# Performance work log

Hardware: AMD Instinct MI355X
Metric: run time of the kernel (lower is better)

The kernel has to match this reference:

```python
import jax, jax.numpy as jnp
import numpy as np

L, H, D, C, V, B, T, BLOCK = 6, 12, 64, 768, 32000, 2, 1024, 2048
EPS = 1e-5


def setup_inputs() -> dict:
    key = jax.random.key(0)
    ks = jax.random.split(key, 21)
    s = 0.02
    n = lambda k, shape: (jax.random.normal(k, shape, dtype=jnp.float32) * s)
    return {
        "x": jax.random.randint(ks[0], (B, T), 0, V),
        "tok_emb": n(ks[1], (V, C)),
        "pos_emb": n(ks[2], (BLOCK, C)),
        "Wq": n(ks[3], (L, H, C, D)),
        "Wk": n(ks[4], (L, H, C, D)),
        "Wv": n(ks[5], (L, H, C, D)),
        "Wo": n(ks[6], (L, H * D, C)),
        "bo": jnp.zeros((L, C), jnp.float32),
        "ln1_g": jnp.ones((L, C), jnp.float32),
        "ln1_b": jnp.zeros((L, C), jnp.float32),
        "ln2_g": jnp.ones((L, C), jnp.float32),
        "ln2_b": jnp.zeros((L, C), jnp.float32),
        "W1": n(ks[7], (L, C, 4 * C)),
        "b1": jnp.zeros((L, 4 * C), jnp.float32),
        "W2": n(ks[8], (L, 4 * C, C)),
        "b2": jnp.zeros((L, C), jnp.float32),
        "lnf_g": jnp.ones((C,), jnp.float32),
        "lnf_b": jnp.zeros((C,), jnp.float32),
        "Wh": n(ks[9], (C, V)),
        "bh": jnp.zeros((V,), jnp.float32),
    }


def _layernorm(x, g, b):
    m = jnp.mean(x, axis=-1, keepdims=True)
    v = jnp.mean(jnp.square(x - m), axis=-1, keepdims=True)
    return (x - m) * jax.lax.rsqrt(v + EPS) * g + b


def _forward(x, tok_emb, pos_emb, Wq, Wk, Wv, Wo, bo, ln1_g, ln1_b, ln2_g, ln2_b,
             W1, b1, W2, b2, lnf_g, lnf_b, Wh, bh):
    h = tok_emb[x] + pos_emb[:T]  # (B,T,C)
    causal = jnp.tril(jnp.ones((T, T), bool))
    scale = C ** (-0.5)  # NOTE: source scales by n_embd**-0.5, not head_size
    for l in range(L):
        a_in = _layernorm(h, ln1_g[l], ln1_b[l])
        q = jnp.einsum('btc,hcd->bhtd', a_in, Wq[l])
        k = jnp.einsum('btc,hcd->bhtd', a_in, Wk[l])
        v = jnp.einsum('btc,hcd->bhtd', a_in, Wv[l])
        scores = jnp.einsum('bhtd,bhsd->bhts', q, k) * scale
        scores = jnp.where(causal, scores, -jnp.inf)
        w = jax.nn.softmax(scores, axis=-1)
        o = jnp.einsum('bhts,bhsd->bhtd', w, v)  # (B,H,T,D)
        o = o.transpose(0, 2, 1, 3).reshape(B, T, H * D)
        h = h + o @ Wo[l] + bo[l]
        f_in = _layernorm(h, ln2_g[l], ln2_b[l])
        h = h + jax.nn.relu(f_in @ W1[l] + b1[l]) @ W2[l] + b2[l]
    h = _layernorm(h, lnf_g, lnf_b)
    return h @ Wh + bh  # logits (B,T,V)


def reference(x, tok_emb, pos_emb, Wq, Wk, Wv, Wo, bo, ln1_g, ln1_b, ln2_g, ln2_b,
              W1, b1, W2, b2, lnf_g, lnf_b, Wh, bh):
    return _forward(x, tok_emb, pos_emb, Wq, Wk, Wv, Wo, bo, ln1_g, ln1_b, ln2_g,
                    ln2_b, W1, b1, W2, b2, lnf_g, lnf_b, Wh, bh)
```

## Files before the change

kernel.cpp:

```cpp
#include <hip/hip_runtime.h>
#include <stdint.h>

typedef unsigned short ushortT;
typedef __bf16 bf16_t;
typedef __bf16 bf16x8 __attribute__((ext_vector_type(8)));
typedef float  f32x4  __attribute__((ext_vector_type(4)));

constexpr int N_LAYER = 6;
constexpr int N_HEAD  = 12;
constexpr int HEAD_D  = 64;
constexpr int N_EMB   = 768;
constexpr int N_VOCAB = 32000;
constexpr int N_B     = 2;
constexpr int N_T     = 1024;
constexpr int N_M     = N_B * N_T;
constexpr int QKVW    = 3 * N_EMB;
constexpr float LN_EPS = 1e-5f;
constexpr float ATT_SCALE = 0.03608439182435161f;

__device__ __forceinline__ float us2f(ushortT u) {
    union { unsigned int i; float f; } c; c.i = ((unsigned int)u) << 16; return c.f;
}
__device__ __forceinline__ ushortT f2b(float f) {
    union { float f; unsigned int u; } c; c.f = f;
    unsigned int u = c.u;
    return (ushortT)((u + 0x7fffu + ((u >> 16) & 1u)) >> 16);
}
__device__ __forceinline__ float ldw(const void* p, int isf, size_t i) {
    if (isf) return ((const float*)p)[i];
    return us2f(((const ushortT*)p)[i]);
}
__device__ __forceinline__ void gload16(const void* g, void* l) {
    __builtin_amdgcn_global_load_lds(
        (const unsigned int __attribute__((address_space(1)))*)g,
        (unsigned int __attribute__((address_space(3)))*)l, 16, 0, 0);
}

__global__ __launch_bounds__(256) void detect_kernel(const unsigned int* __restrict__ w,
                                                     int* __restrict__ flag)
{
    __shared__ int red[256];
    int cnt = 0;
    for (int i = threadIdx.x; i < 4096; i += 256) {
        unsigned int u = w[i];
        float flo = us2f((ushortT)(u & 0xffffu));
        float fhi = us2f((ushortT)(u >> 16));
        if (!(fabsf(flo) < 0.5f)) cnt++;
        if (!(fabsf(fhi) < 0.5f)) cnt++;
    }
    red[threadIdx.x] = cnt;
    __syncthreads();
    for (int off = 128; off > 0; off >>= 1) {
        if (threadIdx.x < off) red[threadIdx.x] += red[threadIdx.x + off];
        __syncthreads();
    }
    if (threadIdx.x == 0) flag[0] = (red[0] > 64) ? 1 : 0;
}

__global__ __launch_bounds__(256) void embed_kernel(const int* __restrict__ x,
        const void* __restrict__ tok, const void* __restrict__ pos,
        const int* __restrict__ flag, float* __restrict__ h)
{
    const int isf = *flag;
    int idx = blockIdx.x * 256 + threadIdx.x;
    if (idx >= N_M * N_EMB) return;
    int m = idx / N_EMB, c = idx - m * N_EMB;
    int t = m & (N_T - 1);
    int tokid = x[m];
    h[idx] = ldw(tok, isf, (size_t)tokid * N_EMB + c) + ldw(pos, isf, (size_t)t * N_EMB + c);
}

__global__ __launch_bounds__(256) void ln_kernel(const float* __restrict__ in,
        const void* __restrict__ g, const void* __restrict__ b, size_t gofs,
        const int* __restrict__ flag, ushortT* __restrict__ outHi, ushortT* __restrict__ outLo)
{
    __shared__ float red[256];
    const int isf = *flag;
    const int tid = threadIdx.x;
    const float* row = in + (size_t)blockIdx.x * N_EMB;
    float v0 = row[tid], v1 = row[tid + 256], v2 = row[tid + 512];
    red[tid] = v0 + v1 + v2;
    __syncthreads();
    for (int off = 128; off > 0; off >>= 1) {
        if (tid < off) red[tid] += red[tid + off];
        __syncthreads();
    }
    float mean = red[0] * (1.0f / N_EMB);
    __syncthreads();
    float d0 = v0 - mean, d1 = v1 - mean, d2 = v2 - mean;
    red[tid] = d0 * d0 + d1 * d1 + d2 * d2;
    __syncthreads();
    for (int off = 128; off > 0; off >>= 1) {
        if (tid < off) red[tid] += red[tid + off];
        __syncthreads();
    }
    float inv = rsqrtf(red[0] * (1.0f / N_EMB) + LN_EPS);
    size_t ob = (size_t)blockIdx.x * N_EMB;
    float dd[3] = {d0, d1, d2};
    #pragma unroll
    for (int e = 0; e < 3; e++) {
        int c = tid + e * 256;
        float v = dd[e] * inv * ldw(g, isf, gofs + c) + ldw(b, isf, gofs + c);
        ushortT hb = f2b(v);
        outHi[ob + c] = hb;
        outLo[ob + c] = f2b(v - us2f(hb));
    }
}

__global__ __launch_bounds__(256) void conv_t(const void* __restrict__ src, size_t sofs,
        const int* __restrict__ flag, ushortT* __restrict__ out, int K, int N)
{
    __shared__ float t[32][33];
    const int isf = *flag;
    const int n0 = blockIdx.x * 32, k0 = blockIdx.y * 32;
    const int tx = threadIdx.x & 31, ty = threadIdx.x >> 5;
    #pragma unroll
    for (int kk = ty; kk < 32; kk += 8)
        t[kk][tx] = ldw(src, isf, sofs + (size_t)(k0 + kk) * N + n0 + tx);
    __syncthreads();
    #pragma unroll
    for (int nn = ty; nn < 32; nn += 8)
        out[(size_t)(n0 + nn) * K + k0 + tx] = f2b(t[tx][nn]);
}

__global__ __launch_bounds__(256) void conv_qkv(const void* __restrict__ Wq,
        const void* __restrict__ Wk, const void* __restrict__ Wv, size_t wofs,
        const int* __restrict__ flag, ushortT* __restrict__ out)
{
    __shared__ float t[32][33];
    const int isf = *flag;
    const int n0 = blockIdx.x * 32, k0 = blockIdx.y * 32;
    const int which = n0 / N_EMB, rem = n0 - which * N_EMB;
    const int h = rem >> 6, d0 = rem & 63;
    const void* src = (which == 0) ? Wq : (which == 1 ? Wk : Wv);
    const size_t base = wofs + (size_t)h * N_EMB * HEAD_D;
    const int tx = threadIdx.x & 31, ty = threadIdx.x >> 5;
    #pragma unroll
    for (int kk = ty; kk < 32; kk += 8)
        t[kk][tx] = ldw(src, isf, base + (size_t)(k0 + kk) * HEAD_D + d0 + tx);
    __syncthreads();
    #pragma unroll
    for (int nn = ty; nn < 32; nn += 8)
        out[(size_t)(n0 + nn) * N_EMB + k0 + tx] = f2b(t[tx][nn]);
}

template<int BM, int BN>
__global__ __launch_bounds__(256, 2) void gemm_mfma(
    const ushortT* __restrict__ Ahi, const ushortT* __restrict__ Alo,
    const ushortT* __restrict__ Bw,
    const void* __restrict__ bias, size_t biasOfs,
    const float* resid,
    float* outF, ushortT* outHi, ushortT* outLo, void* outFinal,
    const int* __restrict__ flag, int Ndim, int K, int relu)
{
    constexpr int MF = BM / 32, NF = BN / 32;
    __shared__ bf16_t Ah[8][BM][8];
    __shared__ bf16_t Al[8][BM][8];
    __shared__ bf16_t Bs[8][BN][8];
    const int tid = threadIdx.x;
    const int lane = tid & 63, w = tid >> 6;
    const int l15 = lane & 15, lg = lane >> 4;
    const int m0 = blockIdx.x * BM, n0 = blockIdx.y * BN;
    const int m_w = (w >> 1) * (BM / 2), n_w = (w & 1) * (BN / 2);
    const int isf = *flag;

    constexpr int CA = BM / 8, CB = BN / 8, TOT = 2 * CA + CB, PW = TOT / 4;

    f32x4 acc[MF][NF];
    #pragma unroll
    for (int i = 0; i < MF; i++)
        #pragma unroll
        for (int j = 0; j < NF; j++) { f32x4 z = {0.f, 0.f, 0.f, 0.f}; acc[i][j] = z; }

    for (int kt = 0; kt < K; kt += 64) {
        __syncthreads();
        #pragma unroll
        for (int q0 = 0; q0 < PW; ++q0) {
            const int q = w * PW + q0;
            const bf16_t* dst; const ushortT* src;
            if (q < CA) {
                const int c = q & 7, hf = q >> 3;
                dst = &Ah[c][hf * 64][0];
                src = Ahi + (size_t)(m0 + hf * 64 + lane) * K + (kt + c * 8);
            } else if (q < 2 * CA) {
                const int qq = q - CA, c = qq & 7, hf = qq >> 3;
                dst = &Al[c][hf * 64][0];
                src = Alo + (size_t)(m0 + hf * 64 + lane) * K + (kt + c * 8);
            } else {
                const int qq = q - 2 * CA, c = qq & 7, hf = qq >> 3;
                dst = &Bs[c][hf * 64][0];
                src = Bw + (size_t)(n0 + hf * 64 + lane) * K + (kt + c * 8);
            }
            gload16((const void*)src, (void*)dst);
        }
        __syncthreads();
        #pragma unroll
        for (int kk = 0; kk < 2; ++kk) {
            const int cb = kk * 4 + lg;
            bf16x8 bv[NF];
            #pragma unroll
            for (int j = 0; j < NF; ++j)
                bv[j] = *(const bf16x8*)(&Bs[cb][n_w + 16 * j + l15][0]);
            #pragma unroll
            for (int i = 0; i < MF; ++i) {
                bf16x8 ah = *(const bf16x8*)(&Ah[cb][m_w + 16 * i + l15][0]);
                bf16x8 al = *(const bf16x8*)(&Al[cb][m_w + 16 * i + l15][0]);
                #pragma unroll
                for (int j = 0; j < NF; ++j) {
                    acc[i][j] = __builtin_amdgcn_mfma_f32_16x16x32_bf16(ah, bv[j], acc[i][j], 0, 0, 0);
                    acc[i][j] = __builtin_amdgcn_mfma_f32_16x16x32_bf16(al, bv[j], acc[i][j], 0, 0, 0);
                }
            }
        }
    }
    #pragma unroll
    for (int i = 0; i < MF; ++i) {
        #pragma unroll
        for (int r = 0; r < 4; ++r) {
            const int row = m0 + m_w + 16 * i + lg * 4 + r;
            const size_t rb = (size_t)row * Ndim;
            #pragma unroll
            for (int j = 0; j < NF; ++j) {
                const int col = n0 + n_w + 16 * j + l15;
                float v = acc[i][j][r];
                if (bias)  v += ldw(bias, isf, biasOfs + col);
                if (resid) v += resid[rb + col];
                if (relu)  v = fmaxf(v, 0.0f);
                if (outF)  outF[rb + col] = v;
                if (outHi) {
                    ushortT hb = f2b(v);
                    outHi[rb + col] = hb;
                    outLo[rb + col] = f2b(v - us2f(hb));
                }
                if (outFinal) {
                    if (isf) ((float*)outFinal)[rb + col] = v;
                    else     ((ushortT*)outFinal)[rb + col] = f2b(v);
                }
            }
        }
    }
}

__global__ __launch_bounds__(256) void attn_kernel(
    const float* __restrict__ qkv, ushortT* __restrict__ oHi, ushortT* __restrict__ oLo)
{
    __shared__ float Qs[64][68];
    __shared__ float KS[64][68];
    __shared__ float Vs[64][68];
    __shared__ float mrow[64], lrow[64], arow[64];
    const int tq = blockIdx.x;
    const int h = blockIdx.y, b = blockIdx.z;
    const int tid = threadIdx.x;
    const int tx = tid & 15, ty = tid >> 4;
    const float* qb = qkv + (size_t)b * N_T * QKVW + h * HEAD_D;
    const float* kb = qb + N_EMB;
    const float* vb = qb + 2 * N_EMB;

    const int rr = tid >> 2;
    const int cc = (tid & 3) * 16;
    {
        const float* src = qb + (size_t)(tq * 64 + rr) * QKVW + cc;
        #pragma unroll
        for (int j = 0; j < 16; j += 4)
            *(float4*)&Qs[rr][cc + j] = *(const float4*)(src + j);
    }
    if (tid < 64) { mrow[tid] = -1e30f; lrow[tid] = 0.0f; }
    float oa[4][4] = {};

    for (int kt = 0; kt <= tq; kt++) {
        __syncthreads();
        {
            const float* ks = kb + (size_t)(kt * 64 + rr) * QKVW + cc;
            const float* vs = vb + (size_t)(kt * 64 + rr) * QKVW + cc;
            #pragma unroll
            for (int j = 0; j < 16; j += 4) {
                *(float4*)&KS[rr][cc + j] = *(const float4*)(ks + j);
                *(float4*)&Vs[rr][cc + j] = *(const float4*)(vs + j);
            }
        }
        __syncthreads();
        float s[4][4] = {};
        #pragma unroll
        for (int kk = 0; kk < 64; kk += 4) {
            float4 qv[4], kv[4];
            #pragma unroll
            for (int i = 0; i < 4; i++) qv[i] = *(const float4*)&Qs[ty * 4 + i][kk];
            #pragma unroll
            for (int j = 0; j < 4; j++) kv[j] = *(const float4*)&KS[tx * 4 + j][kk];
            #pragma unroll
            for (int i = 0; i < 4; i++)
                #pragma unroll
                for (int j = 0; j < 4; j++)
                    s[i][j] += qv[i].x * kv[j].x + qv[i].y * kv[j].y +
                               qv[i].z * kv[j].z + qv[i].w * kv[j].w;
        }
        const int qr0 = tq * 64 + ty * 4, kc0 = kt * 64 + tx * 4;
        #pragma unroll
        for (int i = 0; i < 4; i++)
            #pragma unroll
            for (int j = 0; j < 4; j++)
                s[i][j] = (kc0 + j <= qr0 + i) ? s[i][j] * ATT_SCALE : -1e30f;
        __syncthreads();
        #pragma unroll
        for (int i = 0; i < 4; i++)
            #pragma unroll
            for (int j = 0; j < 4; j++)
                KS[ty * 4 + i][tx * 4 + j] = s[i][j];
        __syncthreads();
        {
            const int r = tid >> 2, part = tid & 3;
            const int c0 = part * 16;
            float mo = mrow[r];
            float mx = -1e30f;
            #pragma unroll
            for (int c = 0; c < 16; c++) mx = fmaxf(mx, KS[r][c0 + c]);
            mx = fmaxf(mx, __shfl_xor(mx, 1));
            mx = fmaxf(mx, __shfl_xor(mx, 2));
            mx = fmaxf(mx, mo);
            float sum = 0.0f;
            #pragma unroll
            for (int c = 0; c < 16; c++) {
                float p = __expf(KS[r][c0 + c] - mx);
                KS[r][c0 + c] = p;
                sum += p;
            }
            sum += __shfl_xor(sum, 1);
            sum += __shfl_xor(sum, 2);
            if (part == 0) {
                float al = __expf(mo - mx);
                mrow[r] = mx;
                lrow[r] = lrow[r] * al + sum;
                arow[r] = al;
            }
        }
        __syncthreads();
        #pragma unroll
        for (int i = 0; i < 4; i++) {
            float al = arow[ty * 4 + i];
            #pragma unroll
            for (int j = 0; j < 4; j++) oa[i][j] *= al;
        }
        #pragma unroll
        for (int ss = 0; ss < 64; ss += 4) {
            float4 p4[4], v4[4];
            #pragma unroll
            for (int i = 0; i < 4; i++) p4[i] = *(const float4*)&KS[ty * 4 + i][ss];
            #pragma unroll
            for (int s2 = 0; s2 < 4; s2++) v4[s2] = *(const float4*)&Vs[ss + s2][tx * 4];
            #pragma unroll
            for (int i = 0; i < 4; i++) {
                float4 P = p4[i];
                oa[i][0] += P.x * v4[0].x + P.y * v4[1].x + P.z * v4[2].x + P.w * v4[3].x;
                oa[i][1] += P.x * v4[0].y + P.y * v4[1].y + P.z * v4[2].y + P.w * v4[3].y;
                oa[i][2] += P.x * v4[0].z + P.y * v4[1].z + P.z * v4[2].z + P.w * v4[3].z;
                oa[i][3] += P.x * v4[0].w + P.y * v4[1].w + P.z * v4[2].w + P.w * v4[3].w;
            }
        }
    }
    #pragma unroll
    for (int i = 0; i < 4; i++) {
        int r = ty * 4 + i;
        int t = tq * 64 + r;
        float invl = 1.0f / lrow[r];
        size_t ob = ((size_t)(b * N_T + t)) * N_EMB + h * HEAD_D + tx * 4;
        #pragma unroll
        for (int jj = 0; jj < 4; jj++) {
            float vv = oa[i][jj] * invl;
            ushortT hb = f2b(vv);
            oHi[ob + jj] = hb;
            oLo[ob + jj] = f2b(vv - us2f(hb));
        }
    }
}

extern "C" void kernel_launch(void* const* d_in, const int* in_sizes, int n_in,
                              void* d_out, int out_size, void* d_ws, size_t ws_size,
                              hipStream_t stream)
{
    const int*  x    = (const int*) d_in[0];
    const void* tok  = d_in[1];
    const void* pos  = d_in[2];
    const void* Wq   = d_in[3];
    const void* Wk   = d_in[4];
    const void* Wv   = d_in[5];
    const void* Wo   = d_in[6];
    const void* bo   = d_in[7];
    const void* ln1g = d_in[8];
    const void* ln1b = d_in[9];
    const void* ln2g = d_in[10];
    const void* ln2b = d_in[11];
    const void* W1   = d_in[12];
    const void* b1   = d_in[13];
    const void* W2   = d_in[14];
    const void* b2   = d_in[15];
    const void* lnfg = d_in[16];
    const void* lnfb = d_in[17];
    const void* Wh   = d_in[18];
    const void* bh   = d_in[19];

    float* ws = (float*)d_ws;
    int* flag = (int*)ws;
    const size_t MC = (size_t)N_M * N_EMB;
    float*   h    = ws + 64;
    ushortT* aHi  = (ushortT*)(h + MC);
    ushortT* aLo  = aHi + MC;
    float*   qkvF = (float*)(aLo + MC);
    ushortT* ffhHi = (ushortT*)qkvF;
    ushortT* ffhLo = ffhHi + 4 * MC;
    ushortT* wstg = (ushortT*)(qkvF + 4 * MC);
    ushortT* wsQ  = wstg;
    ushortT* wsO  = wsQ  + (size_t)QKVW * N_EMB;
    ushortT* wsF1 = wsO  + (size_t)N_EMB * N_EMB;
    ushortT* wsF2 = wsF1 + (size_t)N_EMB * 4 * N_EMB;

    detect_kernel<<<1, 256, 0, stream>>>((const unsigned int*)tok, flag);
    embed_kernel<<<(int)((MC + 255) / 256), 256, 0, stream>>>(x, tok, pos, flag, h);

    for (int l = 0; l < N_LAYER; l++) {
        ln_kernel<<<N_M, 256, 0, stream>>>(h, ln1g, ln1b, (size_t)l * N_EMB, flag, aHi, aLo);

        conv_qkv<<<dim3(QKVW / 32, N_EMB / 32), 256, 0, stream>>>(
            Wq, Wk, Wv, (size_t)l * N_HEAD * N_EMB * HEAD_D, flag, wsQ);
        gemm_mfma<128, 128><<<dim3(N_M / 128, QKVW / 128), 256, 0, stream>>>(
            aHi, aLo, wsQ, nullptr, 0, nullptr, qkvF, nullptr, nullptr, nullptr,
            flag, QKVW, N_EMB, 0);

        attn_kernel<<<dim3(N_T / 64, N_HEAD, N_B), 256, 0, stream>>>(qkvF, aHi, aLo);

        conv_t<<<dim3(N_EMB / 32, N_EMB / 32), 256, 0, stream>>>(
            Wo, (size_t)l * N_EMB * N_EMB, flag, wsO, N_EMB, N_EMB);
        gemm_mfma<64, 64><<<dim3(N_M / 64, N_EMB / 64), 256, 0, stream>>>(
            aHi, aLo, wsO, bo, (size_t)l * N_EMB, h, h, nullptr, nullptr, nullptr,
            flag, N_EMB, N_EMB, 0);

        ln_kernel<<<N_M, 256, 0, stream>>>(h, ln2g, ln2b, (size_t)l * N_EMB, flag, aHi, aLo);

        conv_t<<<dim3(4 * N_EMB / 32, N_EMB / 32), 256, 0, stream>>>(
            W1, (size_t)l * N_EMB * 4 * N_EMB, flag, wsF1, N_EMB, 4 * N_EMB);
        gemm_mfma<128, 128><<<dim3(N_M / 128, 4 * N_EMB / 128), 256, 0, stream>>>(
            aHi, aLo, wsF1, b1, (size_t)l * 4 * N_EMB, nullptr, nullptr, ffhHi, ffhLo, nullptr,
            flag, 4 * N_EMB, N_EMB, 1);

        conv_t<<<dim3(N_EMB / 32, 4 * N_EMB / 32), 256, 0, stream>>>(
            W2, (size_t)l * 4 * N_EMB * N_EMB, flag, wsF2, 4 * N_EMB, N_EMB);
        gemm_mfma<64, 64><<<dim3(N_M / 64, N_EMB / 64), 256, 0, stream>>>(
            ffhHi, ffhLo, wsF2, b2, (size_t)l * N_EMB, h, h, nullptr, nullptr, nullptr,
            flag, N_EMB, 4 * N_EMB, 0);
    }

    ln_kernel<<<N_M, 256, 0, stream>>>(h, lnfg, lnfb, 0, flag, aHi, aLo);

    conv_t<<<dim3(N_VOCAB / 32, N_EMB / 32), 256, 0, stream>>>(
        Wh, 0, flag, wstg, N_EMB, N_VOCAB);
    gemm_mfma<128, 128><<<dim3(N_M / 128, N_VOCAB / 128), 256, 0, stream>>>(
        aHi, aLo, wstg, bh, 0, nullptr, nullptr, nullptr, nullptr, d_out,
        flag, N_VOCAB, N_EMB, 0);
}
```

Before: 5.134 ms.

## Drop split-bf16 activations, double-buffer GEMM, split-K atomics for residual GEMMs

Activations are now stored as a single bf16 tensor instead of a hi/lo pair, which halves the MFMA count and A-operand traffic in every GEMM. The GEMM gains double-buffered LDS staging, a grouped block-index remap, and split-K along grid z, accumulating into the residual with atomicAdd after a separate bias-add kernel. Layernorm reductions switch to wavefront shuffles, and the QKV and FFN1 tiles change to 64x128. Accuracy drops because the low-order correction is removed, and the float atomic accumulation is nondeterministic.

```diff
diff --git a/kernel.cpp b/kernel.cpp
--- a/kernel.cpp
+++ b/kernel.cpp
@@ -72,39 +72,44 @@
 
 __global__ __launch_bounds__(256) void ln_kernel(const float* __restrict__ in,
         const void* __restrict__ g, const void* __restrict__ b, size_t gofs,
-        const int* __restrict__ flag, ushortT* __restrict__ outHi, ushortT* __restrict__ outLo)
-{
-    __shared__ float red[256];
-    const int isf = *flag;
-    const int tid = threadIdx.x;
+        const int* __restrict__ flag, ushortT* __restrict__ out)
+{
+    __shared__ float part[8];
+    const int isf = *flag;
+    const int tid = threadIdx.x, lane = tid & 63, w = tid >> 6;
     const float* row = in + (size_t)blockIdx.x * N_EMB;
     float v0 = row[tid], v1 = row[tid + 256], v2 = row[tid + 512];
-    red[tid] = v0 + v1 + v2;
-    __syncthreads();
-    for (int off = 128; off > 0; off >>= 1) {
-        if (tid < off) red[tid] += red[tid + off];
-        __syncthreads();
-    }
-    float mean = red[0] * (1.0f / N_EMB);
-    __syncthreads();
+    float s = v0 + v1 + v2;
+    #pragma unroll
+    for (int o = 32; o; o >>= 1) s += __shfl_xor(s, o);
+    if (lane == 0) part[w] = s;
+    __syncthreads();
+    float mean = (part[0] + part[1] + part[2] + part[3]) * (1.0f / N_EMB);
     float d0 = v0 - mean, d1 = v1 - mean, d2 = v2 - mean;
-    red[tid] = d0 * d0 + d1 * d1 + d2 * d2;
-    __syncthreads();
-    for (int off = 128; off > 0; off >>= 1) {
-        if (tid < off) red[tid] += red[tid + off];
-        __syncthreads();
-    }
-    float inv = rsqrtf(red[0] * (1.0f / N_EMB) + LN_EPS);
+    float q = d0 * d0 + d1 * d1 + d2 * d2;
+    #pragma unroll
+    for (int o = 32; o; o >>= 1) q += __shfl_xor(q, o);
+    if (lane == 0) part[4 + w] = q;
+    __syncthreads();
+    float inv = rsqrtf((part[4] + part[5] + part[6] + part[7]) * (1.0f / N_EMB) + LN_EPS);
     size_t ob = (size_t)blockIdx.x * N_EMB;
     float dd[3] = {d0, d1, d2};
     #pragma unroll
     for (int e = 0; e < 3; e++) {
         int c = tid + e * 256;
         float v = dd[e] * inv * ldw(g, isf, gofs + c) + ldw(b, isf, gofs + c);
-        ushortT hb = f2b(v);
-        outHi[ob + c] = hb;
-        outLo[ob + c] = f2b(v - us2f(hb));
-    }
+        out[ob + c] = f2b(v);
+    }
+}
+
+__global__ __launch_bounds__(256) void addbias_kernel(float* __restrict__ h,
+        const void* __restrict__ bias, size_t bofs, const int* __restrict__ flag)
+{
+    const int isf = *flag;
+    int idx = blockIdx.x * 256 + threadIdx.x;
+    if (idx >= N_M * N_EMB) return;
+    int m = idx / N_EMB, c = idx - m * N_EMB;
+    h[idx] += ldw(bias, isf, bofs + c);
 }
 
 __global__ __launch_bounds__(256) void conv_t(const void* __restrict__ src, size_t sofs,
@@ -145,74 +150,80 @@
 }
 
 template<int BM, int BN>
-__global__ __launch_bounds__(256, 2) void gemm_mfma(
-    const ushortT* __restrict__ Ahi, const ushortT* __restrict__ Alo,
-    const ushortT* __restrict__ Bw,
+__global__ __launch_bounds__(256) void gemm_mfma(
+    const ushortT* __restrict__ A, const ushortT* __restrict__ Bw,
     const void* __restrict__ bias, size_t biasOfs,
-    const float* resid,
-    float* outF, ushortT* outHi, ushortT* outLo, void* outFinal,
-    const int* __restrict__ flag, int Ndim, int K, int relu)
+    float* __restrict__ outF, ushortT* __restrict__ outH, void* outFinal,
+    float* __restrict__ outAtomic,
+    const int* __restrict__ flag, int Ndim, int K, int kspan, int relu)
 {
     constexpr int MF = BM / 32, NF = BN / 32;
-    __shared__ bf16_t Ah[8][BM][8];
-    __shared__ bf16_t Al[8][BM][8];
-    __shared__ bf16_t Bs[8][BN][8];
+    constexpr int CA = BM / 8, CB = BN / 8, TOT = CA + CB, PW = TOT / 4;
+    __shared__ bf16_t Ah[2][8][BM][8];
+    __shared__ bf16_t Bs[2][8][BN][8];
     const int tid = threadIdx.x;
     const int lane = tid & 63, w = tid >> 6;
     const int l15 = lane & 15, lg = lane >> 4;
-    const int m0 = blockIdx.x * BM, n0 = blockIdx.y * BN;
+
+    const int nxy = gridDim.x * gridDim.y;
+    int id = blockIdx.x + gridDim.x * blockIdx.y;
+    if ((nxy & 7) == 0) {
+        const int per = nxy >> 3;
+        id = (id & 7) * per + (id >> 3);
+    }
+    const int bx = id % gridDim.x, by = id / gridDim.x;
+    const int m0 = bx * BM, n0 = by * BN;
+    const int kt0 = blockIdx.z * kspan;
+    const int nsteps = kspan / 64;
+    const int isf = *flag;
     const int m_w = (w >> 1) * (BM / 2), n_w = (w & 1) * (BN / 2);
-    const int isf = *flag;
-
-    constexpr int CA = BM / 8, CB = BN / 8, TOT = 2 * CA + CB, PW = TOT / 4;
-
-    f32x4 acc[MF][NF];
-    #pragma unroll
-    for (int i = 0; i < MF; i++)
-        #pragma unroll
-        for (int j = 0; j < NF; j++) { f32x4 z = {0.f, 0.f, 0.f, 0.f}; acc[i][j] = z; }
-
-    for (int kt = 0; kt < K; kt += 64) {
-        __syncthreads();
+
+    auto STAGE = [&](int buf, int kt) {
         #pragma unroll
         for (int q0 = 0; q0 < PW; ++q0) {
             const int q = w * PW + q0;
-            const bf16_t* dst; const ushortT* src;
             if (q < CA) {
                 const int c = q & 7, hf = q >> 3;
-                dst = &Ah[c][hf * 64][0];
-                src = Ahi + (size_t)(m0 + hf * 64 + lane) * K + (kt + c * 8);
-            } else if (q < 2 * CA) {
+                gload16(A + (size_t)(m0 + hf * 64 + lane) * K + kt + c * 8,
+                        &Ah[buf][c][hf * 64][0]);
+            } else {
                 const int qq = q - CA, c = qq & 7, hf = qq >> 3;
-                dst = &Al[c][hf * 64][0];
-                src = Alo + (size_t)(m0 + hf * 64 + lane) * K + (kt + c * 8);
-            } else {
-                const int qq = q - 2 * CA, c = qq & 7, hf = qq >> 3;
-                dst = &Bs[c][hf * 64][0];
-                src = Bw + (size_t)(n0 + hf * 64 + lane) * K + (kt + c * 8);
-            }
-            gload16((const void*)src, (void*)dst);
-        }
-        __syncthreads();
+                gload16(Bw + (size_t)(n0 + hf * 64 + lane) * K + kt + c * 8,
+                        &Bs[buf][c][hf * 64][0]);
+            }
+        }
+    };
+
+    f32x4 acc[MF][NF];
+    #pragma unroll
+    for (int i = 0; i < MF; i++)
+        #pragma unroll
+        for (int j = 0; j < NF; j++) { f32x4 z = {0.f, 0.f, 0.f, 0.f}; acc[i][j] = z; }
+
+    STAGE(0, kt0);
+    __syncthreads();
+    int cur = 0;
+    for (int t = 0; t < nsteps; ++t) {
+        if (t + 1 < nsteps) STAGE(cur ^ 1, kt0 + (t + 1) * 64);
         #pragma unroll
         for (int kk = 0; kk < 2; ++kk) {
             const int cb = kk * 4 + lg;
             bf16x8 bv[NF];
             #pragma unroll
             for (int j = 0; j < NF; ++j)
-                bv[j] = *(const bf16x8*)(&Bs[cb][n_w + 16 * j + l15][0]);
+                bv[j] = *(const bf16x8*)(&Bs[cur][cb][n_w + 16 * j + l15][0]);
             #pragma unroll
             for (int i = 0; i < MF; ++i) {
-                bf16x8 ah = *(const bf16x8*)(&Ah[cb][m_w + 16 * i + l15][0]);
-                bf16x8 al = *(const bf16x8*)(&Al[cb][m_w + 16 * i + l15][0]);
+                bf16x8 av = *(const bf16x8*)(&Ah[cur][cb][m_w + 16 * i + l15][0]);
                 #pragma unroll
-                for (int j = 0; j < NF; ++j) {
-                    acc[i][j] = __builtin_amdgcn_mfma_f32_16x16x32_bf16(ah, bv[j], acc[i][j], 0, 0, 0);
-                    acc[i][j] = __builtin_amdgcn_mfma_f32_16x16x32_bf16(al, bv[j], acc[i][j], 0, 0, 0);
-                }
-            }
-        }
-    }
+                for (int j = 0; j < NF; ++j)
+                    acc[i][j] = __builtin_amdgcn_mfma_f32_16x16x32_bf16(av, bv[j], acc[i][j], 0, 0, 0);
+            }
+        }
+        __syncthreads();
+        cur ^= 1;
+    }
+
     #pragma unroll
     for (int i = 0; i < MF; ++i) {
         #pragma unroll
@@ -224,14 +235,10 @@
                 const int col = n0 + n_w + 16 * j + l15;
                 float v = acc[i][j][r];
                 if (bias)  v += ldw(bias, isf, biasOfs + col);
-                if (resid) v += resid[rb + col];
                 if (relu)  v = fmaxf(v, 0.0f);
+                if (outAtomic) atomicAdd(&outAtomic[rb + col], v);
                 if (outF)  outF[rb + col] = v;
-                if (outHi) {
-                    ushortT hb = f2b(v);
-                    outHi[rb + col] = hb;
-                    outLo[rb + col] = f2b(v - us2f(hb));
-                }
+                if (outH)  outH[rb + col] = f2b(v);
                 if (outFinal) {
                     if (isf) ((float*)outFinal)[rb + col] = v;
                     else     ((ushortT*)outFinal)[rb + col] = f2b(v);
@@ -242,7 +249,7 @@
 }
 
 __global__ __launch_bounds__(256) void attn_kernel(
-    const float* __restrict__ qkv, ushortT* __restrict__ oHi, ushortT* __restrict__ oLo)
+    const float* __restrict__ qkv, ushortT* __restrict__ oH)
 {
     __shared__ float Qs[64][68];
     __shared__ float KS[64][68];
@@ -364,12 +371,8 @@
         float invl = 1.0f / lrow[r];
         size_t ob = ((size_t)(b * N_T + t)) * N_EMB + h * HEAD_D + tx * 4;
         #pragma unroll
-        for (int jj = 0; jj < 4; jj++) {
-            float vv = oa[i][jj] * invl;
-            ushortT hb = f2b(vv);
-            oHi[ob + jj] = hb;
-            oLo[ob + jj] = f2b(vv - us2f(hb));
-        }
+        for (int jj = 0; jj < 4; jj++)
+            oH[ob + jj] = f2b(oa[i][jj] * invl);
     }
 }
 
@@ -402,12 +405,10 @@
     int* flag = (int*)ws;
     const size_t MC = (size_t)N_M * N_EMB;
     float*   h    = ws + 64;
-    ushortT* aHi  = (ushortT*)(h + MC);
-    ushortT* aLo  = aHi + MC;
-    float*   qkvF = (float*)(aLo + MC);
-    ushortT* ffhHi = (ushortT*)qkvF;
-    ushortT* ffhLo = ffhHi + 4 * MC;
-    ushortT* wstg = (ushortT*)(qkvF + 4 * MC);
+    ushortT* aH   = (ushortT*)(h + MC);
+    float*   qkvF = (float*)(aH + MC);
+    ushortT* ffh  = (ushortT*)qkvF;
+    ushortT* wstg = (ushortT*)(qkvF + 3 * MC);
     ushortT* wsQ  = wstg;
     ushortT* wsO  = wsQ  + (size_t)QKVW * N_EMB;
     ushortT* wsF1 = wsO  + (size_t)N_EMB * N_EMB;
@@ -416,43 +417,47 @@
     detect_kernel<<<1, 256, 0, stream>>>((const unsigned int*)tok, flag);
     embed_kernel<<<(int)((MC + 255) / 256), 256, 0, stream>>>(x, tok, pos, flag, h);
 
+    const int nb_bias = (int)((MC + 255) / 256);
+
     for (int l = 0; l < N_LAYER; l++) {
-        ln_kernel<<<N_M, 256, 0, stream>>>(h, ln1g, ln1b, (size_t)l * N_EMB, flag, aHi, aLo);
+        ln_kernel<<<N_M, 256, 0, stream>>>(h, ln1g, ln1b, (size_t)l * N_EMB, flag, aH);
 
         conv_qkv<<<dim3(QKVW / 32, N_EMB / 32), 256, 0, stream>>>(
             Wq, Wk, Wv, (size_t)l * N_HEAD * N_EMB * HEAD_D, flag, wsQ);
-        gemm_mfma<128, 128><<<dim3(N_M / 128, QKVW / 128), 256, 0, stream>>>(
-            aHi, aLo, wsQ, nullptr, 0, nullptr, qkvF, nullptr, nullptr, nullptr,
-            flag, QKVW, N_EMB, 0);
-
-        attn_kernel<<<dim3(N_T / 64, N_HEAD, N_B), 256, 0, stream>>>(qkvF, aHi, aLo);
+        gemm_mfma<64, 128><<<dim3(N_M / 64, QKVW / 128), 256, 0, stream>>>(
+            aH, wsQ, nullptr, 0, qkvF, nullptr, nullptr, nullptr,
+            flag, QKVW, N_EMB, N_EMB, 0);
+
+        attn_kernel<<<dim3(N_T / 64, N_HEAD, N_B), 256, 0, stream>>>(qkvF, aH);
 
         conv_t<<<dim3(N_EMB / 32, N_EMB / 32), 256, 0, stream>>>(
             Wo, (size_t)l * N_EMB * N_EMB, flag, wsO, N_EMB, N_EMB);
-        gemm_mfma<64, 64><<<dim3(N_M / 64, N_EMB / 64), 256, 0, stream>>>(
-            aHi, aLo, wsO, bo, (size_t)l * N_EMB, h, h, nullptr, nullptr, nullptr,
-            flag, N_EMB, N_EMB, 0);
-
-        ln_kernel<<<N_M, 256, 0, stream>>>(h, ln2g, ln2b, (size_t)l * N_EMB, flag, aHi, aLo);
+        addbias_kernel<<<nb_bias, 256, 0, stream>>>(h, bo, (size_t)l * N_EMB, flag);
+        gemm_mfma<64, 128><<<dim3(N_M / 64, N_EMB / 128, 3), 256, 0, stream>>>(
+            aH, wsO, nullptr, 0, nullptr, nullptr, nullptr, h,
+            flag, N_EMB, N_EMB, N_EMB / 3, 0);
+
+        ln_kernel<<<N_M, 256, 0, stream>>>(h, ln2g, ln2b, (size_t)l * N_EMB, flag, aH);
 
         conv_t<<<dim3(4 * N_EMB / 32, N_EMB / 32), 256, 0, stream>>>(
             W1, (size_t)l * N_EMB * 4 * N_EMB, flag, wsF1, N_EMB, 4 * N_EMB);
-        gemm_mfma<128, 128><<<dim3(N_M / 128, 4 * N_EMB / 128), 256, 0, stream>>>(
-            aHi, aLo, wsF1, b1, (size_t)l * 4 * N_EMB, nullptr, nullptr, ffhHi, ffhLo, nullptr,
-            flag, 4 * N_EMB, N_EMB, 1);
+        gemm_mfma<64, 128><<<dim3(N_M / 64, 4 * N_EMB / 128), 256, 0, stream>>>(
+            aH, wsF1, b1, (size_t)l * 4 * N_EMB, nullptr, ffh, nullptr, nullptr,
+            flag, 4 * N_EMB, N_EMB, N_EMB, 1);
 
         conv_t<<<dim3(N_EMB / 32, 4 * N_EMB / 32), 256, 0, stream>>>(
             W2, (size_t)l * 4 * N_EMB * N_EMB, flag, wsF2, 4 * N_EMB, N_EMB);
-        gemm_mfma<64, 64><<<dim3(N_M / 64, N_EMB / 64), 256, 0, stream>>>(
-            ffhHi, ffhLo, wsF2, b2, (size_t)l * N_EMB, h, h, nullptr, nullptr, nullptr,
-            flag, N_EMB, 4 * N_EMB, 0);
-    }
-
-    ln_kernel<<<N_M, 256, 0, stream>>>(h, lnfg, lnfb, 0, flag, aHi, aLo);
+        addbias_kernel<<<nb_bias, 256, 0, stream>>>(h, b2, (size_t)l * N_EMB, flag);
+        gemm_mfma<64, 128><<<dim3(N_M / 64, N_EMB / 128, 4), 256, 0, stream>>>(
+            ffh, wsF2, nullptr, 0, nullptr, nullptr, nullptr, h,
+            flag, N_EMB, 4 * N_EMB, N_EMB, 0);
+    }
+
+    ln_kernel<<<N_M, 256, 0, stream>>>(h, lnfg, lnfb, 0, flag, aH);
 
     conv_t<<<dim3(N_VOCAB / 32, N_EMB / 32), 256, 0, stream>>>(
         Wh, 0, flag, wstg, N_EMB, N_VOCAB);
     gemm_mfma<128, 128><<<dim3(N_M / 128, N_VOCAB / 128), 256, 0, stream>>>(
-        aHi, aLo, wstg, bh, 0, nullptr, nullptr, nullptr, nullptr, d_out,
-        flag, N_VOCAB, N_EMB, 0);
-}
+        aH, wstg, bh, 0, nullptr, nullptr, d_out, nullptr,
+        flag, N_VOCAB, N_EMB, N_EMB, 0);
+}
```

Result: faster. 4.363 ms (-15.0%).
